# Performance work log

Hardware: AMD Instinct MI355X
Metric: run time of the kernel (lower is better)

Reference implementation:

```python
import jax, jax.numpy as jnp
import numpy as np

B, N, E, H = 16, 512, 512, 8
D = E // H
NEG = -1e9  # stands in for -inf; other scores are clamped to [-10, 10]


def setup_inputs() -> dict:
    key = jax.random.key(0)
    ks = jax.random.split(key, 11)
    s = 1.0 / np.sqrt(E)
    return {
        "x": jax.random.normal(ks[0], (B, N, E), jnp.float32),
        "db": jax.random.normal(ks[1], (B, N, N), jnp.float32),
        "mask": jax.random.randint(ks[2], (B, N), 0, 2, jnp.int32),
        "wq": jax.random.normal(ks[3], (E, E), jnp.float32) * s,
        "bq": jax.random.normal(ks[4], (E,), jnp.float32) * s,
        "wk": jax.random.normal(ks[5], (E, E), jnp.float32) * s,
        "bk": jax.random.normal(ks[6], (E,), jnp.float32) * s,
        "wv": jax.random.normal(ks[7], (E, E), jnp.float32) * s,
        "bv": jax.random.normal(ks[8], (E,), jnp.float32) * s,
        "wo": jax.random.normal(ks[9], (E, E), jnp.float32) * s,
        "bo": jax.random.normal(ks[10], (E,), jnp.float32) * s,
    }


def reference(x, db, mask, wq, bq, wk, bk, wv, bv, wo, bo):
    # projections -> [B, H, N, D]
    def proj(w, b):
        return (x @ w.T + b).reshape(B, N, H, D).transpose(0, 2, 1, 3)

    q = proj(wq, bq)
    k = proj(wk, bk)
    v = proj(wv, bv)

    scale = 1.0 / np.sqrt(D).astype(np.float32)
    sc = jnp.einsum('bhid,bhjd->bhij', q, k) * scale + db[:, None, :, :]
    sc = jnp.clip(sc, -10.0, 10.0)
    sc = jnp.where(mask[:, None, None, :].astype(bool), sc, NEG)
    a = jax.nn.softmax(sc, axis=-1)  # dropout is identity (p=0 / eval)
    o = jnp.einsum('bhij,bhjd->bhid', a, v)
    o = o.transpose(0, 2, 1, 3).reshape(B, N, E)
    return o @ wo.T + bo
```

## Files before the change

kernel.cpp:

```cpp
#include <hip/hip_runtime.h>

typedef __attribute__((ext_vector_type(8))) short short8;
typedef __attribute__((ext_vector_type(4))) short short4v;
typedef __attribute__((ext_vector_type(4))) float f32x4;

#define MFMA16(A, B, C) __builtin_amdgcn_mfma_f32_16x16x32_bf16(A, B, C, 0, 0, 0)

__device__ __forceinline__ short f2bf(float f) {
    union { float f; unsigned u; } v;
    v.f = f;
    unsigned r = (v.u + 0x7FFFu + ((v.u >> 16) & 1u)) >> 16;
    return (short)r;
}

__device__ __forceinline__ float bf2f(short u) {
    union { unsigned u; float f; } v;
    v.u = ((unsigned)(unsigned short)u) << 16;
    return v.f;
}

__device__ __forceinline__ short8 cvt8(f32x4 a, f32x4 b) {
    unsigned u0, u1, u2, u3;
    asm("v_cvt_pk_bf16_f32 %0, %1, %2" : "=v"(u0) : "v"(a[0]), "v"(a[1]));
    asm("v_cvt_pk_bf16_f32 %0, %1, %2" : "=v"(u1) : "v"(a[2]), "v"(a[3]));
    asm("v_cvt_pk_bf16_f32 %0, %1, %2" : "=v"(u2) : "v"(b[0]), "v"(b[1]));
    asm("v_cvt_pk_bf16_f32 %0, %1, %2" : "=v"(u3) : "v"(b[2]), "v"(b[3]));
    union { unsigned u[4]; short8 s; } r;
    r.u[0] = u0; r.u[1] = u1; r.u[2] = u2; r.u[3] = u3;
    return r.s;
}

__device__ __forceinline__ void cvtpk_store4(short* dst, float p0, float p1,
                                             float p2, float p3) {
    unsigned w01, w23;
    asm("v_cvt_pk_bf16_f32 %0, %1, %2" : "=v"(w01) : "v"(p0), "v"(p1));
    asm("v_cvt_pk_bf16_f32 %0, %1, %2" : "=v"(w23) : "v"(p2), "v"(p3));
    union { unsigned u[2]; short4v s; } r;
    r.u[0] = w01; r.u[1] = w23;
    *(short4v*)dst = r.s;
}

__global__ __launch_bounds__(256) void cvt_all(
    const float* __restrict__ wq, const float* __restrict__ wk,
    const float* __restrict__ wv, const float* __restrict__ wo,
    const float* __restrict__ db, const int* __restrict__ mask,
    short* __restrict__ wcat, short* __restrict__ wob,
    short* __restrict__ dbp) {
    const int blk = blockIdx.x;
    if (blk < 512) {
        int j = blk * 256 + threadIdx.x;
        int w = j >> 15;
        int soff = j & 32767;
        const float* src = (w == 0) ? wq : (w == 1) ? wk : (w == 2) ? wv : wo;
        short* dst;
        int doff;
        if (w < 3) { dst = wcat; doff = j; }
        else       { dst = wob;  doff = soff; }
        const float* p = src + (size_t)soff * 8;
        short8 r;
#pragma unroll
        for (int t = 0; t < 8; ++t) r[t] = f2bf(p[t]);
        *(short8*)(dst + (size_t)doff * 8) = r;
    } else {
        int t = (blk - 512) * 256 + threadIdx.x;
        int f = t * 8;
        int b = f >> 18;
        int rem = f & 262143;
        int qt = rem >> 13;
        int rem2 = rem & 8191;
        int jidx = rem2 >> 10;
        int w = rem2 & 1023;
        int lane = w >> 4;
        int idx0 = w & 15;
        int c = lane & 15, g = lane >> 4;
        int q = qt * 16 + c;
        const float* dbrow = db + ((size_t)b * 512 + q) * 512;
        const int* mrow = mask + b * 512;
        short8 out;
#pragma unroll
        for (int e = 0; e < 8; ++e) {
            int idx = idx0 + e;
            int nt = idx >> 2, r = idx & 3;
            int j = jidx * 64 + nt * 16 + g * 4 + r;
            float val = (mrow[j] != 0) ? dbrow[j] : -1e9f;
            out[e] = f2bf(val);
        }
        *(short8*)(dbp + (size_t)f) = out;
    }
}

__global__ __launch_bounds__(256) void qkv128(
    const float* __restrict__ X, const short* __restrict__ Bw,
    const float* __restrict__ bq, const float* __restrict__ bk,
    const float* __restrict__ bv, short* __restrict__ qo,
    short* __restrict__ ko, short* __restrict__ vto) {
    __shared__ short As[128 * 72];
    __shared__ short Bs[128 * 72];
    const int tid = threadIdx.x, lane = tid & 63, wid = tid >> 6;
    const int c = lane & 15, g = lane >> 4;
    const int wr = (wid >> 1) * 64, wc = (wid & 1) * 64;
    const int m0 = blockIdx.x * 128, e0 = blockIdx.y * 128;

    const f32x4 Z = {0.f, 0.f, 0.f, 0.f};
    f32x4 acc[4][4];
#pragma unroll
    for (int i = 0; i < 4; ++i)
#pragma unroll
        for (int j = 0; j < 4; ++j) acc[i][j] = Z;

    short8 pa[4], pb[4];
#pragma unroll
    for (int p = 0; p < 4; ++p) {
        int u = p * 256 + tid;
        int row = u >> 3, c8 = u & 7;
        const float* xs = &X[(size_t)(m0 + row) * 512 + c8 * 8];
        pa[p] = cvt8(*(const f32x4*)xs, *(const f32x4*)(xs + 4));
        pb[p] = *(const short8*)&Bw[(size_t)(e0 + row) * 512 + c8 * 8];
    }
    for (int it = 0; it < 8; ++it) {
        __syncthreads();
#pragma unroll
        for (int p = 0; p < 4; ++p) {
            int u = p * 256 + tid;
            int row = u >> 3, c8 = u & 7;
            *(short8*)&As[row * 72 + c8 * 8] = pa[p];
            *(short8*)&Bs[row * 72 + c8 * 8] = pb[p];
        }
        if (it < 7) {
            int k0 = (it + 1) * 64;
#pragma unroll
            for (int p = 0; p < 4; ++p) {
                int u = p * 256 + tid;
                int row = u >> 3, c8 = u & 7;
                const float* xs = &X[(size_t)(m0 + row) * 512 + k0 + c8 * 8];
                pa[p] = cvt8(*(const f32x4*)xs, *(const f32x4*)(xs + 4));
                pb[p] = *(const short8*)&Bw[(size_t)(e0 + row) * 512 + k0 + c8 * 8];
            }
        }
        __syncthreads();
#pragma unroll
        for (int ks = 0; ks < 2; ++ks) {
            short8 af[4], bf[4];
#pragma unroll
            for (int mt = 0; mt < 4; ++mt)
                af[mt] = *(const short8*)&As[(wr + mt * 16 + c) * 72 + ks * 32 + g * 8];
#pragma unroll
            for (int nt = 0; nt < 4; ++nt)
                bf[nt] = *(const short8*)&Bs[(wc + nt * 16 + c) * 72 + ks * 32 + g * 8];
#pragma unroll
            for (int mt = 0; mt < 4; ++mt)
#pragma unroll
                for (int nt = 0; nt < 4; ++nt)
                    acc[mt][nt] = MFMA16(af[mt], bf[nt], acc[mt][nt]);
        }
    }

    const int z = e0 >> 9;
    const float* bp = (z == 0) ? bq : (z == 1) ? bk : bv;
    if (z < 2) {
        short* out = (z == 0) ? qo : ko;
#pragma unroll
        for (int nt = 0; nt < 4; ++nt) {
            int eh = (e0 & 511) + wc + nt * 16 + c;
            float bsv = bp[eh];
            int h = eh >> 6, d = eh & 63;
#pragma unroll
            for (int mt = 0; mt < 4; ++mt)
#pragma unroll
                for (int r = 0; r < 4; ++r) {
                    int m = m0 + wr + mt * 16 + g * 4 + r;
                    int bb = m >> 9, n = m & 511;
                    out[(((size_t)bb * 8 + h) * 512 + n) * 64 + d] =
                        f2bf(acc[mt][nt][r] + bsv);
                }
        }
    } else {
#pragma unroll
        for (int nt = 0; nt < 4; ++nt) {
            int eh = (e0 & 511) + wc + nt * 16 + c;
            float bsv = bp[eh];
            int h = eh >> 6, d = eh & 63;
#pragma unroll
            for (int mt = 0; mt < 4; ++mt) {
                int m = m0 + wr + mt * 16 + g * 4;
                int bb = m >> 9, n = m & 511;
                short4v w;
#pragma unroll
                for (int r = 0; r < 4; ++r) w[r] = f2bf(acc[mt][nt][r] + bsv);
                *(short4v*)&vto[(((size_t)bb * 8 + h) * 64 + d) * 512 + n] = w;
            }
        }
    }
}

__global__ __launch_bounds__(256) void out128(const short* __restrict__ A,
                                              const short* __restrict__ W,
                                              const float* __restrict__ bo,
                                              float* __restrict__ out) {
    __shared__ short As[128 * 72];
    __shared__ short Bs[128 * 72];
    const int tid = threadIdx.x, lane = tid & 63, wid = tid >> 6;
    const int c = lane & 15, g = lane >> 4;
    const int wr = (wid >> 1) * 64, wc = (wid & 1) * 64;
    const int m0 = blockIdx.x * 128, e0 = blockIdx.y * 128;

    const f32x4 Z = {0.f, 0.f, 0.f, 0.f};
    f32x4 acc[4][4];
#pragma unroll
    for (int i = 0; i < 4; ++i)
#pragma unroll
        for (int j = 0; j < 4; ++j) acc[i][j] = Z;

    short8 pa[4], pb[4];
#pragma unroll
    for (int p = 0; p < 4; ++p) {
        int u = p * 256 + tid;
        int row = u >> 3, c8 = u & 7;
        pa[p] = *(const short8*)&A[(size_t)(m0 + row) * 512 + c8 * 8];
        pb[p] = *(const short8*)&W[(size_t)(e0 + row) * 512 + c8 * 8];
    }
    for (int it = 0; it < 8; ++it) {
        __syncthreads();
#pragma unroll
        for (int p = 0; p < 4; ++p) {
            int u = p * 256 + tid;
            int row = u >> 3, c8 = u & 7;
            *(short8*)&As[row * 72 + c8 * 8] = pa[p];
            *(short8*)&Bs[row * 72 + c8 * 8] = pb[p];
        }
        if (it < 7) {
            int k0 = (it + 1) * 64;
#pragma unroll
            for (int p = 0; p < 4; ++p) {
                int u = p * 256 + tid;
                int row = u >> 3, c8 = u & 7;
                pa[p] = *(const short8*)&A[(size_t)(m0 + row) * 512 + k0 + c8 * 8];
                pb[p] = *(const short8*)&W[(size_t)(e0 + row) * 512 + k0 + c8 * 8];
            }
        }
        __syncthreads();
#pragma unroll
        for (int ks = 0; ks < 2; ++ks) {
            short8 af[4], bf[4];
#pragma unroll
            for (int mt = 0; mt < 4; ++mt)
                af[mt] = *(const short8*)&As[(wr + mt * 16 + c) * 72 + ks * 32 + g * 8];
#pragma unroll
            for (int nt = 0; nt < 4; ++nt)
                bf[nt] = *(const short8*)&Bs[(wc + nt * 16 + c) * 72 + ks * 32 + g * 8];
#pragma unroll
            for (int mt = 0; mt < 4; ++mt)
#pragma unroll
                for (int nt = 0; nt < 4; ++nt)
                    acc[mt][nt] = MFMA16(af[mt], bf[nt], acc[mt][nt]);
        }
    }

#pragma unroll
    for (int nt = 0; nt < 4; ++nt) {
        int e = e0 + wc + nt * 16 + c;
        float bsv = bo[e];
#pragma unroll
        for (int mt = 0; mt < 4; ++mt)
#pragma unroll
            for (int r = 0; r < 4; ++r) {
                int m = m0 + wr + mt * 16 + g * 4 + r;
                out[(size_t)m * 512 + e] = acc[mt][nt][r] + bsv;
            }
    }
}

__global__ __launch_bounds__(256, 2) void attn_mfma(
    const short* __restrict__ q, const short* __restrict__ k,
    const short* __restrict__ vt, const short* __restrict__ dbp_all,
    short* __restrict__ o) {
    __shared__ short Ks[2][64 * 72];
    __shared__ short Vs[2][64 * 72];
    __shared__ short pl[8][16 * 72];
    const int tid = threadIdx.x;
    const int lane = tid & 63, wid = tid >> 6;
    const int c = lane & 15, g = lane >> 4;
    const int f = blockIdx.x;
    const int blo = f & 7;
    const int t = f >> 3;
    const int u4 = t & 3;
    const int h = (t >> 2) & 7;
    const int b = (t >> 5) * 8 + blo;
    const int u = u4 * 4 + wid;
    const int q0A = u * 32;

    const short* kp = k + (((size_t)b * 8 + h) * 512) * 64;
    const short* vp = vt + (((size_t)b * 8 + h) * 64) * 512;
    const short* qpA = q + (((size_t)b * 8 + h) * 512 + q0A) * 64;
    const short* dbpA = dbp_all + (((size_t)b * 32 + u * 2) * 8) * 1024 + lane * 16;
    const short* dbpB = dbpA + 8192;

    const int s0 = tid * 2, s1 = tid * 2 + 1;
    const int kr0 = s0 >> 3, kc0 = (s0 & 7) * 8;
    const int kr1 = s1 >> 3, kc1 = (s1 & 7) * 8;

    short8 qA0 = *(const short8*)&qpA[c * 64 + g * 8];
    short8 qA1 = *(const short8*)&qpA[c * 64 + 32 + g * 8];
    short8 qB0 = *(const short8*)&qpA[(16 + c) * 64 + g * 8];
    short8 qB1 = *(const short8*)&qpA[(16 + c) * 64 + 32 + g * 8];

    {
        short8 k0v = *(const short8*)&kp[kr0 * 64 + kc0];
        short8 k1v = *(const short8*)&kp[kr1 * 64 + kc1];
        short8 v0v = *(const short8*)&vp[kr0 * 512 + kc0];
        short8 v1v = *(const short8*)&vp[kr1 * 512 + kc1];
        *(short8*)&Ks[0][kr0 * 72 + kc0] = k0v;
        *(short8*)&Ks[0][kr1 * 72 + kc1] = k1v;
        *(short8*)&Vs[0][kr0 * 72 + kc0] = v0v;
        *(short8*)&Vs[0][kr1 * 72 + kc1] = v1v;
    }
    short8 dA0 = *(const short8*)&dbpA[0];
    short8 dA1 = *(const short8*)&dbpA[8];
    short8 dB0 = *(const short8*)&dbpB[0];
    short8 dB1 = *(const short8*)&dbpB[8];
    __syncthreads();

    const f32x4 Z = {0.f, 0.f, 0.f, 0.f};
    f32x4 oA[4], oB[4];
    float lsA[4], lsB[4];
#pragma unroll
    for (int dt = 0; dt < 4; ++dt) { oA[dt] = Z; oB[dt] = Z; }
#pragma unroll
    for (int nt = 0; nt < 4; ++nt) { lsA[nt] = 0.f; lsB[nt] = 0.f; }

    short* plA = &pl[wid * 2][0];
    short* plB = &pl[wid * 2 + 1][0];

    for (int jidx = 0; jidx < 8; ++jidx) {
        const int cur = jidx & 1;
        const int j0 = jidx * 64;
        short8 kn0, kn1, vn0, vn1;
        if (jidx < 7) {
            const int jn = j0 + 64;
            kn0 = *(const short8*)&kp[(jn + kr0) * 64 + kc0];
            kn1 = *(const short8*)&kp[(jn + kr1) * 64 + kc1];
            vn0 = *(const short8*)&vp[kr0 * 512 + jn + kc0];
            vn1 = *(const short8*)&vp[kr1 * 512 + jn + kc1];
        }
        short8 kf0, kf1;
        f32x4 sA[4], sB[4];
#pragma unroll
        for (int nt = 0; nt < 4; ++nt) {
            kf0 = *(const short8*)&Ks[cur][(nt * 16 + c) * 72 + g * 8];
            kf1 = *(const short8*)&Ks[cur][(nt * 16 + c) * 72 + 32 + g * 8];
            f32x4 zA = Z, zB = Z;
            __builtin_amdgcn_s_setprio(1);
            zA = MFMA16(kf0, qA0, zA);
            zB = MFMA16(kf0, qB0, zB);
            zA = MFMA16(kf1, qA1, zA);
            zB = MFMA16(kf1, qB1, zB);
            __builtin_amdgcn_s_setprio(0);
            sA[nt] = zA;
            sB[nt] = zB;
        }
#pragma unroll
        for (int nt = 0; nt < 4; ++nt) {
            float pp0, pp1, pp2, pp3;
            {
                int idx = nt * 4;
                float d0 = bf2f(idx < 8 ? dA0[idx] : dA1[idx - 8]);
                float d1 = bf2f(idx + 1 < 8 ? dA0[idx + 1] : dA1[idx - 7]);
                float d2 = bf2f(idx + 2 < 8 ? dA0[idx + 2] : dA1[idx - 6]);
                float d3 = bf2f(idx + 3 < 8 ? dA0[idx + 3] : dA1[idx - 5]);
                float v0 = fminf(fmaxf(fmaf(sA[nt][0], 0.125f, d0), -10.f), 10.f);
                float v1 = fminf(fmaxf(fmaf(sA[nt][1], 0.125f, d1), -10.f), 10.f);
                float v2 = fminf(fmaxf(fmaf(sA[nt][2], 0.125f, d2), -10.f), 10.f);
                float v3 = fminf(fmaxf(fmaf(sA[nt][3], 0.125f, d3), -10.f), 10.f);
                pp0 = exp2f(fmaf(v0, 1.442695041f, -14.42695041f));
                pp1 = exp2f(fmaf(v1, 1.442695041f, -14.42695041f));
                pp2 = exp2f(fmaf(v2, 1.442695041f, -14.42695041f));
                pp3 = exp2f(fmaf(v3, 1.442695041f, -14.42695041f));
            }
            lsA[nt] += (pp0 + pp1) + (pp2 + pp3);
            cvtpk_store4(&plA[c * 72 + nt * 16 + g * 4], pp0, pp1, pp2, pp3);
        }
        if (jidx < 7) {
            dA0 = *(const short8*)&dbpA[(jidx + 1) * 1024];
            dA1 = *(const short8*)&dbpA[(jidx + 1) * 1024 + 8];
        }
#pragma unroll
        for (int nt = 0; nt < 4; ++nt) {
            float pp0, pp1, pp2, pp3;
            {
                int idx = nt * 4;
                float d0 = bf2f(idx < 8 ? dB0[idx] : dB1[idx - 8]);
                float d1 = bf2f(idx + 1 < 8 ? dB0[idx + 1] : dB1[idx - 7]);
                float d2 = bf2f(idx + 2 < 8 ? dB0[idx + 2] : dB1[idx - 6]);
                float d3 = bf2f(idx + 3 < 8 ? dB0[idx + 3] : dB1[idx - 5]);
                float v0 = fminf(fmaxf(fmaf(sB[nt][0], 0.125f, d0), -10.f), 10.f);
                float v1 = fminf(fmaxf(fmaf(sB[nt][1], 0.125f, d1), -10.f), 10.f);
                float v2 = fminf(fmaxf(fmaf(sB[nt][2], 0.125f, d2), -10.f), 10.f);
                float v3 = fminf(fmaxf(fmaf(sB[nt][3], 0.125f, d3), -10.f), 10.f);
                pp0 = exp2f(fmaf(v0, 1.442695041f, -14.42695041f));
                pp1 = exp2f(fmaf(v1, 1.442695041f, -14.42695041f));
                pp2 = exp2f(fmaf(v2, 1.442695041f, -14.42695041f));
                pp3 = exp2f(fmaf(v3, 1.442695041f, -14.42695041f));
            }
            lsB[nt] += (pp0 + pp1) + (pp2 + pp3);
            cvtpk_store4(&plB[c * 72 + nt * 16 + g * 4], pp0, pp1, pp2, pp3);
        }
        if (jidx < 7) {
            dB0 = *(const short8*)&dbpB[(jidx + 1) * 1024];
            dB1 = *(const short8*)&dbpB[(jidx + 1) * 1024 + 8];
        }
        asm volatile("s_waitcnt lgkmcnt(0)" ::: "memory");
        __builtin_amdgcn_sched_barrier(0);
        short8 pA0 = *(const short8*)&plA[c * 72 + g * 8];
        short8 pA1 = *(const short8*)&plA[c * 72 + 32 + g * 8];
        short8 pB0 = *(const short8*)&plB[c * 72 + g * 8];
        short8 pB1 = *(const short8*)&plB[c * 72 + 32 + g * 8];
#pragma unroll
        for (int dt = 0; dt < 4; ++dt) {
            short8 vf0 = *(const short8*)&Vs[cur][(dt * 16 + c) * 72 + g * 8];
            short8 vf1 = *(const short8*)&Vs[cur][(dt * 16 + c) * 72 + 32 + g * 8];
            __builtin_amdgcn_s_setprio(1);
            oA[dt] = MFMA16(vf0, pA0, oA[dt]);
            oB[dt] = MFMA16(vf0, pB0, oB[dt]);
            oA[dt] = MFMA16(vf1, pA1, oA[dt]);
            oB[dt] = MFMA16(vf1, pB1, oB[dt]);
            __builtin_amdgcn_s_setprio(0);
        }
        if (jidx < 7) {
            const int nxt = cur ^ 1;
            *(short8*)&Ks[nxt][kr0 * 72 + kc0] = kn0;
            *(short8*)&Ks[nxt][kr1 * 72 + kc1] = kn1;
            *(short8*)&Vs[nxt][kr0 * 72 + kc0] = vn0;
            *(short8*)&Vs[nxt][kr1 * 72 + kc1] = vn1;
            __syncthreads();
        }
    }
    float lA = (lsA[0] + lsA[1]) + (lsA[2] + lsA[3]);
    lA += __shfl_xor(lA, 16);
    lA += __shfl_xor(lA, 32);
    float lB = (lsB[0] + lsB[1]) + (lsB[2] + lsB[3]);
    lB += __shfl_xor(lB, 16);
    lB += __shfl_xor(lB, 32);
    const float invA = 1.f / lA, invB = 1.f / lB;
#pragma unroll
    for (int dt = 0; dt < 4; ++dt) {
        short4v wa, wb;
#pragma unroll
        for (int r = 0; r < 4; ++r) {
            wa[r] = f2bf(oA[dt][r] * invA);
            wb[r] = f2bf(oB[dt][r] * invB);
        }
        *(short4v*)&o[((size_t)b * 512 + q0A + c) * 512 + h * 64 + dt * 16 + g * 4] = wa;
        *(short4v*)&o[((size_t)b * 512 + q0A + 16 + c) * 512 + h * 64 + dt * 16 + g * 4] = wb;
    }
}

extern "C" void kernel_launch(void* const* d_in, const int* in_sizes, int n_in,
                              void* d_out, int out_size, void* d_ws, size_t ws_size,
                              hipStream_t stream) {
    const float* x  = (const float*)d_in[0];
    const float* db = (const float*)d_in[1];
    const int* msk  = (const int*)d_in[2];
    const float* wq = (const float*)d_in[3];
    const float* bq = (const float*)d_in[4];
    const float* wk = (const float*)d_in[5];
    const float* bk = (const float*)d_in[6];
    const float* wv = (const float*)d_in[7];
    const float* bv = (const float*)d_in[8];
    const float* wo = (const float*)d_in[9];
    const float* bo = (const float*)d_in[10];
    float* out = (float*)d_out;

    short* wcat = (short*)d_ws;
    short* wob  = wcat + 786432;
    short* qb   = wob + 262144;
    short* kb   = qb + 4194304;
    short* vtb  = kb + 4194304;
    short* ob   = vtb + 4194304;
    short* dbp  = ob + 4194304;

    cvt_all<<<2560, 256, 0, stream>>>(wq, wk, wv, wo, db, msk, wcat, wob, dbp);
    qkv128<<<dim3(64, 12), 256, 0, stream>>>(x, wcat, bq, bk, bv, qb, kb, vtb);
    attn_mfma<<<512, 256, 0, stream>>>(qb, kb, vtb, dbp, ob);
    out128<<<dim3(64, 4), 256, 0, stream>>>(ob, wob, bo, out);
}
```

Measured before the change: 74.52 us.

## Split weight conversion and fuse bias-mask prep into QKV projection launch

Weight conversion to bf16 moves into its own small kernel. The db/mask conversion into the MFMA-ordered bf16 bias goes into the QKV projection kernel as extra blocks, using a flattened 1D grid. This lets the bandwidth-bound bias packing run at the same time as the compute-bound GEMM blocks instead of in front of them. The trade-off is that the fused kernel reserves shared memory for every block, including the bias-packing blocks that never use it, which may limit occupancy for those blocks.

```diff
diff --git a/kernel.cpp b/kernel.cpp
--- a/kernel.cpp
+++ b/kernel.cpp
@@ -40,29 +40,39 @@
     *(short4v*)dst = r.s;
 }
 
-__global__ __launch_bounds__(256) void cvt_all(
+__global__ __launch_bounds__(256) void cvt_w(
     const float* __restrict__ wq, const float* __restrict__ wk,
     const float* __restrict__ wv, const float* __restrict__ wo,
-    const float* __restrict__ db, const int* __restrict__ mask,
-    short* __restrict__ wcat, short* __restrict__ wob,
+    short* __restrict__ wcat, short* __restrict__ wob) {
+    int j = blockIdx.x * 256 + threadIdx.x;
+    int w = j >> 15;
+    int soff = j & 32767;
+    const float* src = (w == 0) ? wq : (w == 1) ? wk : (w == 2) ? wv : wo;
+    short* dst;
+    int doff;
+    if (w < 3) { dst = wcat; doff = j; }
+    else       { dst = wob;  doff = soff; }
+    const float* p = src + (size_t)soff * 8;
+    short8 r;
+#pragma unroll
+    for (int t = 0; t < 8; ++t) r[t] = f2bf(p[t]);
+    *(short8*)(dst + (size_t)doff * 8) = r;
+}
+
+__global__ __launch_bounds__(256) void qkv_db(
+    const float* __restrict__ X, const short* __restrict__ Bw,
+    const float* __restrict__ bq, const float* __restrict__ bk,
+    const float* __restrict__ bv, const float* __restrict__ db,
+    const int* __restrict__ mask, short* __restrict__ qo,
+    short* __restrict__ ko, short* __restrict__ vto,
     short* __restrict__ dbp) {
-    const int blk = blockIdx.x;
-    if (blk < 512) {
-        int j = blk * 256 + threadIdx.x;
-        int w = j >> 15;
-        int soff = j & 32767;
-        const float* src = (w == 0) ? wq : (w == 1) ? wk : (w == 2) ? wv : wo;
-        short* dst;
-        int doff;
-        if (w < 3) { dst = wcat; doff = j; }
-        else       { dst = wob;  doff = soff; }
-        const float* p = src + (size_t)soff * 8;
-        short8 r;
-#pragma unroll
-        for (int t = 0; t < 8; ++t) r[t] = f2bf(p[t]);
-        *(short8*)(dst + (size_t)doff * 8) = r;
-    } else {
-        int t = (blk - 512) * 256 + threadIdx.x;
+    __shared__ short As[128 * 72];
+    __shared__ short Bs[128 * 72];
+    const int gb = blockIdx.x;
+    const int tid = threadIdx.x;
+
+    if (gb >= 768) {
+        int t = (gb - 768) * 256 + tid;
         int f = t * 8;
         int b = f >> 18;
         int rem = f & 262143;
@@ -86,20 +96,13 @@
             out[e] = f2bf(val);
         }
         *(short8*)(dbp + (size_t)f) = out;
-    }
-}
-
-__global__ __launch_bounds__(256) void qkv128(
-    const float* __restrict__ X, const short* __restrict__ Bw,
-    const float* __restrict__ bq, const float* __restrict__ bk,
-    const float* __restrict__ bv, short* __restrict__ qo,
-    short* __restrict__ ko, short* __restrict__ vto) {
-    __shared__ short As[128 * 72];
-    __shared__ short Bs[128 * 72];
-    const int tid = threadIdx.x, lane = tid & 63, wid = tid >> 6;
+        return;
+    }
+
+    const int lane = tid & 63, wid = tid >> 6;
     const int c = lane & 15, g = lane >> 4;
     const int wr = (wid >> 1) * 64, wc = (wid & 1) * 64;
-    const int m0 = blockIdx.x * 128, e0 = blockIdx.y * 128;
+    const int m0 = (gb & 63) * 128, e0 = (gb >> 6) * 128;
 
     const f32x4 Z = {0.f, 0.f, 0.f, 0.f};
     f32x4 acc[4][4];
@@ -478,8 +481,9 @@
     short* ob   = vtb + 4194304;
     short* dbp  = ob + 4194304;
 
-    cvt_all<<<2560, 256, 0, stream>>>(wq, wk, wv, wo, db, msk, wcat, wob, dbp);
-    qkv128<<<dim3(64, 12), 256, 0, stream>>>(x, wcat, bq, bk, bv, qb, kb, vtb);
+    cvt_w<<<512, 256, 0, stream>>>(wq, wk, wv, wo, wcat, wob);
+    qkv_db<<<2816, 256, 0, stream>>>(x, wcat, bq, bk, bv, db, msk,
+                                     qb, kb, vtb, dbp);
     attn_mfma<<<512, 256, 0, stream>>>(qb, kb, vtb, dbp, ob);
     out128<<<dim3(64, 4), 256, 0, stream>>>(ob, wob, bo, out);
 }
```

Result: slower. 77.12 us (+3.5%).

## Fuse bias/mask preprocessing into attention kernel, reading fp32 bias directly

Applied to the files above, without the earlier changes.

Drops the separate pass that converted the fp32 attention bias and mask into a pre-swizzled bf16 buffer. The attention kernel now reads fp32 bias rows directly, converts them to bf16 in registers, and applies the mask through per-block ballot bitmasks, setting masked scores to a low constant before the exponent. This removes one full write and re-read of a B×N×N intermediate. In exchange, every head block re-reads the fp32 bias (8 heads share it) at twice the bytes per element, and the inner loop gains masking ALU work.

```diff
diff --git a/kernel.cpp b/kernel.cpp
--- a/kernel.cpp
+++ b/kernel.cpp
@@ -40,53 +40,23 @@
     *(short4v*)dst = r.s;
 }
 
-__global__ __launch_bounds__(256) void cvt_all(
+__global__ __launch_bounds__(256) void cvt_w(
     const float* __restrict__ wq, const float* __restrict__ wk,
     const float* __restrict__ wv, const float* __restrict__ wo,
-    const float* __restrict__ db, const int* __restrict__ mask,
-    short* __restrict__ wcat, short* __restrict__ wob,
-    short* __restrict__ dbp) {
-    const int blk = blockIdx.x;
-    if (blk < 512) {
-        int j = blk * 256 + threadIdx.x;
-        int w = j >> 15;
-        int soff = j & 32767;
-        const float* src = (w == 0) ? wq : (w == 1) ? wk : (w == 2) ? wv : wo;
-        short* dst;
-        int doff;
-        if (w < 3) { dst = wcat; doff = j; }
-        else       { dst = wob;  doff = soff; }
-        const float* p = src + (size_t)soff * 8;
-        short8 r;
-#pragma unroll
-        for (int t = 0; t < 8; ++t) r[t] = f2bf(p[t]);
-        *(short8*)(dst + (size_t)doff * 8) = r;
-    } else {
-        int t = (blk - 512) * 256 + threadIdx.x;
-        int f = t * 8;
-        int b = f >> 18;
-        int rem = f & 262143;
-        int qt = rem >> 13;
-        int rem2 = rem & 8191;
-        int jidx = rem2 >> 10;
-        int w = rem2 & 1023;
-        int lane = w >> 4;
-        int idx0 = w & 15;
-        int c = lane & 15, g = lane >> 4;
-        int q = qt * 16 + c;
-        const float* dbrow = db + ((size_t)b * 512 + q) * 512;
-        const int* mrow = mask + b * 512;
-        short8 out;
-#pragma unroll
-        for (int e = 0; e < 8; ++e) {
-            int idx = idx0 + e;
-            int nt = idx >> 2, r = idx & 3;
-            int j = jidx * 64 + nt * 16 + g * 4 + r;
-            float val = (mrow[j] != 0) ? dbrow[j] : -1e9f;
-            out[e] = f2bf(val);
-        }
-        *(short8*)(dbp + (size_t)f) = out;
-    }
+    short* __restrict__ wcat, short* __restrict__ wob) {
+    int j = blockIdx.x * 256 + threadIdx.x;
+    int w = j >> 15;
+    int soff = j & 32767;
+    const float* src = (w == 0) ? wq : (w == 1) ? wk : (w == 2) ? wv : wo;
+    short* dst;
+    int doff;
+    if (w < 3) { dst = wcat; doff = j; }
+    else       { dst = wob;  doff = soff; }
+    const float* p = src + (size_t)soff * 8;
+    short8 r;
+#pragma unroll
+    for (int t = 0; t < 8; ++t) r[t] = f2bf(p[t]);
+    *(short8*)(dst + (size_t)doff * 8) = r;
 }
 
 __global__ __launch_bounds__(256) void qkv128(
@@ -272,8 +242,8 @@
 
 __global__ __launch_bounds__(256, 2) void attn_mfma(
     const short* __restrict__ q, const short* __restrict__ k,
-    const short* __restrict__ vt, const short* __restrict__ dbp_all,
-    short* __restrict__ o) {
+    const short* __restrict__ vt, const float* __restrict__ db,
+    const int* __restrict__ mask, short* __restrict__ o) {
     __shared__ short Ks[2][64 * 72];
     __shared__ short Vs[2][64 * 72];
     __shared__ short pl[8][16 * 72];
@@ -292,8 +262,14 @@
     const short* kp = k + (((size_t)b * 8 + h) * 512) * 64;
     const short* vp = vt + (((size_t)b * 8 + h) * 64) * 512;
     const short* qpA = q + (((size_t)b * 8 + h) * 512 + q0A) * 64;
-    const short* dbpA = dbp_all + (((size_t)b * 32 + u * 2) * 8) * 1024 + lane * 16;
-    const short* dbpB = dbpA + 8192;
+    const float* dbA = db + ((size_t)b * 512 + q0A + c) * 512 + g * 4;
+    const float* dbB = dbA + (size_t)16 * 512;
+    const int* mp = mask + b * 512;
+
+    unsigned long long mm[8];
+#pragma unroll
+    for (int jj = 0; jj < 8; ++jj)
+        mm[jj] = __ballot(mp[jj * 64 + lane] != 0);
 
     const int s0 = tid * 2, s1 = tid * 2 + 1;
     const int kr0 = s0 >> 3, kc0 = (s0 & 7) * 8;
@@ -314,10 +290,15 @@
         *(short8*)&Vs[0][kr0 * 72 + kc0] = v0v;
         *(short8*)&Vs[0][kr1 * 72 + kc1] = v1v;
     }
-    short8 dA0 = *(const short8*)&dbpA[0];
-    short8 dA1 = *(const short8*)&dbpA[8];
-    short8 dB0 = *(const short8*)&dbpB[0];
-    short8 dB1 = *(const short8*)&dbpB[8];
+    short8 dA0, dA1, dB0, dB1;
+    {
+        f32x4 a0 = *(const f32x4*)&dbA[0],  a1 = *(const f32x4*)&dbA[16];
+        f32x4 a2 = *(const f32x4*)&dbA[32], a3 = *(const f32x4*)&dbA[48];
+        dA0 = cvt8(a0, a1); dA1 = cvt8(a2, a3);
+        f32x4 b0 = *(const f32x4*)&dbB[0],  b1 = *(const f32x4*)&dbB[16];
+        f32x4 b2 = *(const f32x4*)&dbB[32], b3 = *(const f32x4*)&dbB[48];
+        dB0 = cvt8(b0, b1); dB1 = cvt8(b2, b3);
+    }
     __syncthreads();
 
     const f32x4 Z = {0.f, 0.f, 0.f, 0.f};
@@ -342,6 +323,7 @@
             vn0 = *(const short8*)&vp[kr0 * 512 + jn + kc0];
             vn1 = *(const short8*)&vp[kr1 * 512 + jn + kc1];
         }
+        const unsigned long long sh = mm[jidx] >> (g * 4);
         short8 kf0, kf1;
         f32x4 sA[4], sB[4];
 #pragma unroll
@@ -371,6 +353,10 @@
                 float v1 = fminf(fmaxf(fmaf(sA[nt][1], 0.125f, d1), -10.f), 10.f);
                 float v2 = fminf(fmaxf(fmaf(sA[nt][2], 0.125f, d2), -10.f), 10.f);
                 float v3 = fminf(fmaxf(fmaf(sA[nt][3], 0.125f, d3), -10.f), 10.f);
+                v0 = ((sh >> (nt * 16 + 0)) & 1ull) ? v0 : -30.f;
+                v1 = ((sh >> (nt * 16 + 1)) & 1ull) ? v1 : -30.f;
+                v2 = ((sh >> (nt * 16 + 2)) & 1ull) ? v2 : -30.f;
+                v3 = ((sh >> (nt * 16 + 3)) & 1ull) ? v3 : -30.f;
                 pp0 = exp2f(fmaf(v0, 1.442695041f, -14.42695041f));
                 pp1 = exp2f(fmaf(v1, 1.442695041f, -14.42695041f));
                 pp2 = exp2f(fmaf(v2, 1.442695041f, -14.42695041f));
@@ -380,8 +366,10 @@
             cvtpk_store4(&plA[c * 72 + nt * 16 + g * 4], pp0, pp1, pp2, pp3);
         }
         if (jidx < 7) {
-            dA0 = *(const short8*)&dbpA[(jidx + 1) * 1024];
-            dA1 = *(const short8*)&dbpA[(jidx + 1) * 1024 + 8];
+            const float* pA = dbA + (jidx + 1) * 64;
+            f32x4 a0 = *(const f32x4*)&pA[0],  a1 = *(const f32x4*)&pA[16];
+            f32x4 a2 = *(const f32x4*)&pA[32], a3 = *(const f32x4*)&pA[48];
+            dA0 = cvt8(a0, a1); dA1 = cvt8(a2, a3);
         }
 #pragma unroll
         for (int nt = 0; nt < 4; ++nt) {
@@ -396,6 +384,10 @@
                 float v1 = fminf(fmaxf(fmaf(sB[nt][1], 0.125f, d1), -10.f), 10.f);
                 float v2 = fminf(fmaxf(fmaf(sB[nt][2], 0.125f, d2), -10.f), 10.f);
                 float v3 = fminf(fmaxf(fmaf(sB[nt][3], 0.125f, d3), -10.f), 10.f);
+                v0 = ((sh >> (nt * 16 + 0)) & 1ull) ? v0 : -30.f;
+                v1 = ((sh >> (nt * 16 + 1)) & 1ull) ? v1 : -30.f;
+                v2 = ((sh >> (nt * 16 + 2)) & 1ull) ? v2 : -30.f;
+                v3 = ((sh >> (nt * 16 + 3)) & 1ull) ? v3 : -30.f;
                 pp0 = exp2f(fmaf(v0, 1.442695041f, -14.42695041f));
                 pp1 = exp2f(fmaf(v1, 1.442695041f, -14.42695041f));
                 pp2 = exp2f(fmaf(v2, 1.442695041f, -14.42695041f));
@@ -405,8 +397,10 @@
             cvtpk_store4(&plB[c * 72 + nt * 16 + g * 4], pp0, pp1, pp2, pp3);
         }
         if (jidx < 7) {
-            dB0 = *(const short8*)&dbpB[(jidx + 1) * 1024];
-            dB1 = *(const short8*)&dbpB[(jidx + 1) * 1024 + 8];
+            const float* pB = dbB + (jidx + 1) * 64;
+            f32x4 b0 = *(const f32x4*)&pB[0],  b1 = *(const f32x4*)&pB[16];
+            f32x4 b2 = *(const f32x4*)&pB[32], b3 = *(const f32x4*)&pB[48];
+            dB0 = cvt8(b0, b1); dB1 = cvt8(b2, b3);
         }
         asm volatile("s_waitcnt lgkmcnt(0)" ::: "memory");
         __builtin_amdgcn_sched_barrier(0);
@@ -476,10 +470,9 @@
     short* kb   = qb + 4194304;
     short* vtb  = kb + 4194304;
     short* ob   = vtb + 4194304;
-    short* dbp  = ob + 4194304;
-
-    cvt_all<<<2560, 256, 0, stream>>>(wq, wk, wv, wo, db, msk, wcat, wob, dbp);
+
+    cvt_w<<<512, 256, 0, stream>>>(wq, wk, wv, wo, wcat, wob);
     qkv128<<<dim3(64, 12), 256, 0, stream>>>(x, wcat, bq, bk, bv, qb, kb, vtb);
-    attn_mfma<<<512, 256, 0, stream>>>(qb, kb, vtb, dbp, ob);
+    attn_mfma<<<512, 256, 0, stream>>>(qb, kb, vtb, db, msk, ob);
     out128<<<dim3(64, 4), 256, 0, stream>>>(ob, wob, bo, out);
 }
```

After: 73.11 us. No clear change (-1.9%).
